# Optimization experiments

Measured on AMD Instinct MI355X. Metric: run time of the kernel, lower is better.

## Reference

```python
import jax, jax.numpy as jnp
import numpy as np

D = 2048          # in_features == out_features (d_model)
H_TOTAL = 8192    # hidden_features, split across experts
E = 8             # num_experts
K = 2             # num_selects (top-k)
HE = H_TOTAL // E # per-expert hidden size
B, S = 2, 2048


def setup_inputs() -> dict:
    key = jax.random.key(0)
    ks = jax.random.split(key, 8)
    scale_up = 1.0 / np.sqrt(D)
    scale_dn = 1.0 / np.sqrt(HE)
    return {
        "x": jax.random.normal(ks[0], (B, S, D), dtype=jnp.float32),
        # mlp gate network: Linear(D,E,no bias) -> tanh -> Linear(E,E,no bias)
        "Wg1": jax.random.normal(ks[1], (E, D), dtype=jnp.float32) * 0.02,
        "Wg2": jax.random.normal(ks[2], (E, E), dtype=jnp.float32) * 0.2,
        # per-expert GLU-MLP weights (stacked over expert axis)
        "Wup": jax.random.uniform(ks[3], (E, HE, D), dtype=jnp.float32, minval=-scale_up, maxval=scale_up),
        "bup": jax.random.uniform(ks[4], (E, HE), dtype=jnp.float32, minval=-scale_up, maxval=scale_up),
        "Wdown": jax.random.uniform(ks[5], (E, D, HE), dtype=jnp.float32, minval=-scale_dn, maxval=scale_dn),
        "bdown": jax.random.uniform(ks[6], (E, D), dtype=jnp.float32, minval=-scale_dn, maxval=scale_dn),
    }


def reference(x, Wg1, Wg2, Wup, bup, Wdown, bdown):
    Bd, Sd, Dd = x.shape
    T = Bd * Sd
    xt = x.reshape(T, Dd)                                   # [T, D] tokens

    # ---- TopKBalancedNoisyGate (eval mode: no noise) ----
    logits = jnp.tanh(xt @ Wg1.T) @ Wg2.T                   # [T, E]
    _, top_idx = jax.lax.top_k(logits, K)                   # [T, K]
    top_logits = jnp.take_along_axis(logits, top_idx, axis=1)
    top_scores = jax.nn.softmax(top_logits.astype(jnp.float32), axis=1).astype(logits.dtype)
    # scatter top-k scores into dense [T, E] (zeros elsewhere)
    rows = jnp.arange(T)[:, None]
    scores = jnp.zeros_like(logits).at[rows, top_idx].set(top_scores)

    # ---- per-expert Linear-GLU experts: up -> silu -> down, score-combined ----
    up = jnp.einsum('td,ehd->teh', xt, Wup) + bup           # [T, E, HE]
    h = jax.nn.silu(up)
    down = jnp.einsum('teh,eoh->teo', h, Wdown) + bdown     # [T, E, D]
    out = jnp.einsum('te,teo->to', scores, down)            # [T, D]
    return out.reshape(Bd, Sd, Dd)
```

## Files before the change

kernel.cpp:

```cpp
#include <hip/hip_runtime.h>
#include <hip/hip_bf16.h>

#define D_DIM 2048
#define HE_DIM 1024
#define E_NUM 8
#define T_NUM 4096
#define TK_NUM 8192
#define TILE 128
#define BK 64
#define MAXROWS 9216
#define MAXMT 72

#define M_CNT(e)  ((e) * 32)
#define M_FILL(e) (256 + (e) * 32)
#define M_OFF  512
#define M_NMT  520
#define M_TE   528
#define M_TB   600
#define M_TICKET 704
#define M_INTS 1024

typedef unsigned short u16;
typedef __attribute__((ext_vector_type(8))) short bf16x8;
typedef __attribute__((ext_vector_type(4))) float f32x4;

#define OFF_XB   ((size_t)0)
#define OFF_WUPB (OFF_XB + (size_t)T_NUM * D_DIM * 2)
#define OFF_SLOT ((size_t)0)
#define OFF_WDNB (OFF_WUPB + (size_t)E_NUM * HE_DIM * D_DIM * 2)
#define OFF_H    (OFF_WDNB + (size_t)E_NUM * D_DIM * HE_DIM * 2)
#define OFF_SCR  (OFF_H + (size_t)MAXROWS * HE_DIM * 2)
#define OFF_EIDX (OFF_SCR + (size_t)TK_NUM * 4)
#define OFF_RT   (OFF_EIDX + (size_t)TK_NUM * 4)
#define OFF_RS   (OFF_RT + (size_t)MAXROWS * 4)
#define OFF_META (OFF_RS + (size_t)MAXROWS * 4)

__device__ __forceinline__ u16 f2bf(float f) {
  unsigned u = __float_as_uint(f);
  u += 0x7FFFu + ((u >> 16) & 1u);
  return (u16)(u >> 16);
}
__device__ __forceinline__ float bf_lo(unsigned u) { return __uint_as_float(u << 16); }
__device__ __forceinline__ float bf_hi(unsigned u) { return __uint_as_float(u & 0xFFFF0000u); }

__device__ __forceinline__ void gload16(const void* g, void* l) {
  __builtin_amdgcn_global_load_lds((const __attribute__((address_space(1))) void*)g,
                                   (__attribute__((address_space(3))) void*)l,
                                   16, 0, 0);
}

#define WAIT_VM4 asm volatile("s_waitcnt vmcnt(4)" ::: "memory")
#define WAIT_VM0 asm volatile("s_waitcnt vmcnt(0)" ::: "memory")
#define SBAR     { __builtin_amdgcn_s_barrier(); asm volatile("" ::: "memory"); }

__global__ void k_cvt2(const float4* __restrict__ s1, const float4* __restrict__ s2,
                       ushort4* __restrict__ d1, ushort4* __restrict__ d2, int n4,
                       int* __restrict__ meta, int* __restrict__ rows_slot,
                       float* __restrict__ rowscore) {
  const int i0 = blockIdx.x * blockDim.x + threadIdx.x;
  if (i0 < M_INTS) meta[i0] = 0;
  if (i0 < MAXROWS) { rows_slot[i0] = -1; rowscore[i0] = 0.0f; }
  const int st = gridDim.x * blockDim.x;
  for (int i = i0; i < 2 * n4; i += st) {
    const float4* s = (i < n4) ? s1 : s2;
    ushort4* d = (i < n4) ? d1 : d2;
    int j = (i < n4) ? i : i - n4;
    float4 v = s[j];
    ushort4 o;
    o.x = f2bf(v.x); o.y = f2bf(v.y); o.z = f2bf(v.z); o.w = f2bf(v.w);
    d[j] = o;
  }
}

__global__ __launch_bounds__(256) void k_gate(
    const float4* __restrict__ x4, const float4* __restrict__ Wg1_4,
    const float* __restrict__ Wg2, ushort4* __restrict__ xb4,
    int* __restrict__ eidx, float* __restrict__ scr, int* __restrict__ meta) {
  __shared__ float4 wg1s[E_NUM * (D_DIM / 4)];
  __shared__ int cnt_s[E_NUM];
  __shared__ int lastf;
  const int tid = threadIdx.x;
  if (tid < E_NUM) cnt_s[tid] = 0;
#pragma unroll
  for (int i = 0; i < 16; ++i) wg1s[tid + i * 256] = Wg1_4[tid + i * 256];
  __syncthreads();

  const int w = tid >> 6;
  const int lane = tid & 63;
  for (int j = 0; j < 4; ++j) {
    const int t = blockIdx.x * 16 + w * 4 + j;
    float acc[E_NUM];
#pragma unroll
    for (int e = 0; e < E_NUM; ++e) acc[e] = 0.f;
#pragma unroll
    for (int i = 0; i < 8; ++i) {
      const int c = lane + i * 64;
      float4 xv = x4[(size_t)t * 512 + c];
      ushort4 o;
      o.x = f2bf(xv.x); o.y = f2bf(xv.y); o.z = f2bf(xv.z); o.w = f2bf(xv.w);
      xb4[(size_t)t * 512 + c] = o;
#pragma unroll
      for (int e = 0; e < E_NUM; ++e) {
        float4 wv = wg1s[e * 512 + c];
        acc[e] += xv.x * wv.x + xv.y * wv.y + xv.z * wv.z + xv.w * wv.w;
      }
    }
#pragma unroll
    for (int e = 0; e < E_NUM; ++e) {
      float v = acc[e];
#pragma unroll
      for (int off = 32; off; off >>= 1) v += __shfl_xor(v, off, 64);
      acc[e] = v;
    }
    if (lane == 0) {
      float l1[E_NUM], lg[E_NUM];
#pragma unroll
      for (int e = 0; e < E_NUM; ++e) l1[e] = tanhf(acc[e]);
#pragma unroll
      for (int i = 0; i < E_NUM; ++i) {
        float s = 0.f;
#pragma unroll
        for (int e = 0; e < E_NUM; ++e) s += l1[e] * Wg2[i * E_NUM + e];
        lg[i] = s;
      }
      int i0 = 0; float v0 = lg[0];
#pragma unroll
      for (int i = 1; i < E_NUM; ++i) if (lg[i] > v0) { v0 = lg[i]; i0 = i; }
      int i1 = -1; float v1 = -3.4e38f;
#pragma unroll
      for (int i = 0; i < E_NUM; ++i) if (i != i0 && lg[i] > v1) { v1 = lg[i]; i1 = i; }
      float e1 = __expf(v1 - v0);
      float s0 = 1.f / (1.f + e1);
      float s1 = e1 * s0;
      eidx[t * 2] = i0; eidx[t * 2 + 1] = i1;
      scr[t * 2] = s0;  scr[t * 2 + 1] = s1;
      atomicAdd(&cnt_s[i0], 1);
      atomicAdd(&cnt_s[i1], 1);
    }
  }
  __syncthreads();
  if (tid < E_NUM) atomicAdd(&meta[M_CNT(tid)], cnt_s[tid]);

  if (tid == 0) {
    __threadfence();
    lastf = (atomicAdd(&meta[M_TICKET], 1) == (int)gridDim.x - 1);
  }
  __syncthreads();
  if (lastf && tid < 64) {
    const int l2 = tid;
    int cnt = (l2 < E_NUM) ? atomicAdd(&meta[M_CNT(l2)], 0) : 0;
    int tiles = (cnt + TILE - 1) / TILE;
    int pre = tiles;
#pragma unroll
    for (int off = 1; off < E_NUM; off <<= 1) {
      int v = __shfl_up(pre, off, 64);
      if (l2 >= off && l2 < E_NUM) pre += v;
    }
    int tb_excl = pre - tiles;
    if (l2 < E_NUM) meta[M_OFF + l2] = tb_excl * TILE;
    const int nmt = __shfl(pre, E_NUM - 1, 64);
    if (l2 == 0) meta[M_NMT] = nmt;
    int tb[E_NUM];
#pragma unroll
    for (int k = 0; k < E_NUM; ++k) tb[k] = __shfl(tb_excl, k, 64);
    for (int mt = l2; mt < nmt; mt += 64) {
      int e = 0;
#pragma unroll
      for (int k = 1; k < E_NUM; ++k) if (mt >= tb[k]) e = k;
      meta[M_TE + mt] = e;
      meta[M_TB + mt] = mt * TILE;
    }
  }
}

__global__ void k_assign(const int* __restrict__ eidx, const float* __restrict__ scr,
                         int* __restrict__ meta, int* __restrict__ rows_slot,
                         float* __restrict__ rowscore) {
  int i = blockIdx.x * blockDim.x + threadIdx.x;
  const int lane = threadIdx.x & 63;
  int e = eidx[i];
  int pos = 0;
#pragma unroll
  for (int ex = 0; ex < E_NUM; ++ex) {
    unsigned long long m = __ballot(e == ex);
    if (e == ex) {
      int leader = __ffsll((long long)m) - 1;
      int rank = __popcll(m & ((1ull << lane) - 1ull));
      int b = 0;
      if (lane == leader) b = atomicAdd(&meta[M_FILL(ex)], __popcll(m));
      b = __shfl(b, leader, 64);
      pos = b + rank;
    }
  }
  int r = meta[M_OFF + e] + pos;
  rows_slot[r] = i;
  rowscore[r] = scr[i];
}

__global__ __launch_bounds__(512) void k_up(
    const u16* __restrict__ xb, const u16* __restrict__ wupb,
    const float* __restrict__ bup, const int* __restrict__ meta,
    const int* __restrict__ rows_slot, u16* __restrict__ hbuf) {
  const int mt = blockIdx.y;
  if (mt >= meta[M_NMT]) return;
  const int e = meta[M_TE + mt];
  const int mbase = meta[M_TB + mt];
  const int nt = blockIdx.x;

  __shared__ u16 As[3][TILE * BK];
  __shared__ u16 Bs[3][TILE * BK];

  const int tid = threadIdx.x;
  const int lane = tid & 63;
  const int w = tid >> 6;
  const int r0 = tid >> 3;
  const int cb = (((tid & 7) ^ (r0 & 7)) * 8);

  const u16* gA[2];
  const u16* gB[2];
#pragma unroll
  for (int j = 0; j < 2; ++j) {
    int s = rows_slot[mbase + r0 + 64 * j]; if (s < 0) s = 0;
    gA[j] = xb + (size_t)(s >> 1) * D_DIM + cb;
    gB[j] = wupb + ((size_t)e * HE_DIM + nt * TILE + r0 + 64 * j) * D_DIM + cb;
  }

  const int wm = (w & 1) * 64;
  const int wn = (w >> 1) * 32;
  const int quad = lane >> 4;
  const int l16 = lane & 15;
  const int sw = l16 & 7;

  f32x4 acc[4][2] = {};

#define STAGE_UP(buf, k0) \
  { gload16(gA[0] + (k0), &As[buf][tid * 8]);        \
    gload16(gA[1] + (k0), &As[buf][tid * 8 + 4096]); \
    gload16(gB[0] + (k0), &Bs[buf][tid * 8]);        \
    gload16(gB[1] + (k0), &Bs[buf][tid * 8 + 4096]); }

  STAGE_UP(0, 0);
  STAGE_UP(1, BK);
  WAIT_VM4;
  SBAR;
  int cur = 0, nxt = 2;
  for (int k0 = 0; k0 < D_DIM; k0 += BK) {
    const bool pf = (k0 + 2 * BK < D_DIM);
    if (pf) STAGE_UP(nxt, k0 + 2 * BK);
    const u16* pa0 = &As[cur][(wm + l16) * BK];
    const u16* pb0 = &Bs[cur][(wn + l16) * BK];
#pragma unroll
    for (int h = 0; h < 2; ++h) {
      const int off = ((h * 4 + quad) ^ sw) * 8;
      bf16x8 af[4], bfr[2];
#pragma unroll
      for (int i = 0; i < 4; ++i) af[i] = *(const bf16x8*)(pa0 + i * 16 * BK + off);
#pragma unroll
      for (int i = 0; i < 2; ++i) bfr[i] = *(const bf16x8*)(pb0 + i * 16 * BK + off);
#pragma unroll
      for (int mi = 0; mi < 4; ++mi)
#pragma unroll
        for (int ni = 0; ni < 2; ++ni)
          acc[mi][ni] = __builtin_amdgcn_mfma_f32_16x16x32_bf16(af[mi], bfr[ni], acc[mi][ni], 0, 0, 0);
    }
    if (pf) { WAIT_VM4; } else { WAIT_VM0; }
    SBAR;
    cur = (cur == 2) ? 0 : cur + 1;
    nxt = (nxt == 2) ? 0 : nxt + 1;
  }

#pragma unroll
  for (int mi = 0; mi < 4; ++mi) {
    const int m = wm + mi * 16 + quad * 4;
#pragma unroll
    for (int ni = 0; ni < 2; ++ni) {
      const int ng = nt * TILE + wn + ni * 16 + l16;
      const float bias = bup[e * HE_DIM + ng];
#pragma unroll
      for (int r = 0; r < 4; ++r) {
        float v = acc[mi][ni][r] + bias;
        v = v / (1.0f + __expf(-v));
        hbuf[(size_t)(mbase + m + r) * HE_DIM + ng] = f2bf(v);
      }
    }
  }
}

__global__ __launch_bounds__(512) void k_down(
    const u16* __restrict__ hbuf, const u16* __restrict__ wdnb,
    const float* __restrict__ bdown, const int* __restrict__ meta,
    const int* __restrict__ rows_slot, const float* __restrict__ rowscore,
    u16* __restrict__ slot) {
  const int mt = blockIdx.y;
  if (mt >= meta[M_NMT]) return;
  const int e = meta[M_TE + mt];
  const int mbase = meta[M_TB + mt];
  const int nt = blockIdx.x;

  __shared__ u16 As[3][TILE * BK];
  __shared__ u16 Bs[3][TILE * BK];

  const int tid = threadIdx.x;
  const int lane = tid & 63;
  const int w = tid >> 6;
  const int r0 = tid >> 3;
  const int cb = (((tid & 7) ^ (r0 & 7)) * 8);

  const u16* gA[2];
  const u16* gB[2];
#pragma unroll
  for (int j = 0; j < 2; ++j) {
    gA[j] = hbuf + (size_t)(mbase + r0 + 64 * j) * HE_DIM + cb;
    gB[j] = wdnb + ((size_t)e * D_DIM + nt * TILE + r0 + 64 * j) * HE_DIM + cb;
  }

  const int wm = (w & 1) * 64;
  const int wn = (w >> 1) * 32;
  const int quad = lane >> 4;
  const int l16 = lane & 15;
  const int sw = l16 & 7;

  f32x4 acc[4][2] = {};

#define STAGE_DN(buf, k0) \
  { gload16(gA[0] + (k0), &As[buf][tid * 8]);        \
    gload16(gA[1] + (k0), &As[buf][tid * 8 + 4096]); \
    gload16(gB[0] + (k0), &Bs[buf][tid * 8]);        \
    gload16(gB[1] + (k0), &Bs[buf][tid * 8 + 4096]); }

  STAGE_DN(0, 0);
  STAGE_DN(1, BK);
  WAIT_VM4;
  SBAR;
  int cur = 0, nxt = 2;
  for (int k0 = 0; k0 < HE_DIM; k0 += BK) {
    const bool pf = (k0 + 2 * BK < HE_DIM);
    if (pf) STAGE_DN(nxt, k0 + 2 * BK);
    const u16* pa0 = &As[cur][(wm + l16) * BK];
    const u16* pb0 = &Bs[cur][(wn + l16) * BK];
#pragma unroll
    for (int h = 0; h < 2; ++h) {
      const int off = ((h * 4 + quad) ^ sw) * 8;
      bf16x8 af[4], bfr[2];
#pragma unroll
      for (int i = 0; i < 4; ++i) af[i] = *(const bf16x8*)(pa0 + i * 16 * BK + off);
#pragma unroll
      for (int i = 0; i < 2; ++i) bfr[i] = *(const bf16x8*)(pb0 + i * 16 * BK + off);
#pragma unroll
      for (int mi = 0; mi < 4; ++mi)
#pragma unroll
        for (int ni = 0; ni < 2; ++ni)
          acc[mi][ni] = __builtin_amdgcn_mfma_f32_16x16x32_bf16(af[mi], bfr[ni], acc[mi][ni], 0, 0, 0);
    }
    if (pf) { WAIT_VM4; } else { WAIT_VM0; }
    SBAR;
    cur = (cur == 2) ? 0 : cur + 1;
    nxt = (nxt == 2) ? 0 : nxt + 1;
  }

#pragma unroll
  for (int mi = 0; mi < 4; ++mi) {
    const int m = wm + mi * 16 + quad * 4;
#pragma unroll
    for (int r = 0; r < 4; ++r) {
      const int rg = mbase + m + r;
      const int s = rows_slot[rg];
      const float sc = rowscore[rg];
      if (s < 0) continue;
      u16* dst = slot + (size_t)s * D_DIM;
#pragma unroll
      for (int ni = 0; ni < 2; ++ni) {
        const int ng = nt * TILE + wn + ni * 16 + l16;
        float v = (acc[mi][ni][r] + bdown[e * D_DIM + ng]) * sc;
        dst[ng] = f2bf(v);
      }
    }
  }
}

__global__ __launch_bounds__(256) void k_combine(const u16* __restrict__ slot,
                                                 float* __restrict__ out) {
  int i = blockIdx.x * blockDim.x + threadIdx.x;
  int t = i >> 8;
  int c = i & 255;
  const uint4* p0 = (const uint4*)(slot + (size_t)(t * 2) * D_DIM) + c;
  const uint4* p1 = (const uint4*)(slot + (size_t)(t * 2 + 1) * D_DIM) + c;
  uint4 a = *p0, b = *p1;
  float4 o0, o1;
  o0.x = bf_lo(a.x) + bf_lo(b.x);  o0.y = bf_hi(a.x) + bf_hi(b.x);
  o0.z = bf_lo(a.y) + bf_lo(b.y);  o0.w = bf_hi(a.y) + bf_hi(b.y);
  o1.x = bf_lo(a.z) + bf_lo(b.z);  o1.y = bf_hi(a.z) + bf_hi(b.z);
  o1.z = bf_lo(a.w) + bf_lo(b.w);  o1.w = bf_hi(a.w) + bf_hi(b.w);
  float4* po = (float4*)(out + (size_t)t * D_DIM) + c * 2;
  po[0] = o0;
  po[1] = o1;
}

extern "C" void kernel_launch(void* const* d_in, const int* in_sizes, int n_in,
                              void* d_out, int out_size, void* d_ws, size_t ws_size,
                              hipStream_t stream) {
  const float* x     = (const float*)d_in[0];
  const float* Wg1   = (const float*)d_in[1];
  const float* Wg2   = (const float*)d_in[2];
  const float* Wup   = (const float*)d_in[3];
  const float* bup   = (const float*)d_in[4];
  const float* Wdown = (const float*)d_in[5];
  const float* bdown = (const float*)d_in[6];
  float* out = (float*)d_out;

  char* ws = (char*)d_ws;
  u16*   xb         = (u16*)(ws + OFF_XB);
  u16*   wupb       = (u16*)(ws + OFF_WUPB);
  u16*   wdnb       = (u16*)(ws + OFF_WDNB);
  u16*   hbuf       = (u16*)(ws + OFF_H);
  u16*   slotbuf    = (u16*)(ws + OFF_SLOT);
  float* scr        = (float*)(ws + OFF_SCR);
  int*   eidx       = (int*)(ws + OFF_EIDX);
  int*   rows_slot  = (int*)(ws + OFF_RT);
  float* rowscore   = (float*)(ws + OFF_RS);
  int*   meta       = (int*)(ws + OFF_META);

  k_cvt2<<<8192, 256, 0, stream>>>((const float4*)Wup, (const float4*)Wdown,
                                   (ushort4*)wupb, (ushort4*)wdnb,
                                   E_NUM * HE_DIM * D_DIM / 4,
                                   meta, rows_slot, rowscore);
  k_gate<<<T_NUM / 16, 256, 0, stream>>>((const float4*)x, (const float4*)Wg1, Wg2,
                                         (ushort4*)xb, eidx, scr, meta);
  k_assign<<<TK_NUM / 256, 256, 0, stream>>>(eidx, scr, meta, rows_slot, rowscore);
  k_up<<<dim3(HE_DIM / TILE, MAXMT), 512, 0, stream>>>(xb, wupb, bup, meta, rows_slot, hbuf);
  k_down<<<dim3(D_DIM / TILE, MAXMT), 512, 0, stream>>>(hbuf, wdnb, bdown, meta,
                                                        rows_slot, rowscore, slotbuf);
  k_combine<<<T_NUM * D_DIM / 8 / 256, 256, 0, stream>>>(slotbuf, out);
}
```

Before: 420.7 us.

## Use 4-wave blocks with 64x64 warp tiles and BK=32 in expert GEMMs

Both expert GEMM kernels go from 8 waves to 4 waves per 128x128 block, so each wave now computes a 64x64 sub-tile (4x4 MFMAs) instead of 64x32. The K step drops from 64 to 32, the global-to-LDS loader is remapped for 256 threads with a matching 4-way XOR swizzle, and s_setprio is raised around the MFMA burst. The aim is more register-level reuse per fragment load, less LDS traffic per FLOP, and smaller LDS footprint for higher occupancy. In exchange there are twice as many loop iterations and barriers per K, and higher accumulator register pressure.

```diff
diff --git a/kernel.cpp b/kernel.cpp
--- a/kernel.cpp
+++ b/kernel.cpp
@@ -7,7 +7,7 @@
 #define T_NUM 4096
 #define TK_NUM 8192
 #define TILE 128
-#define BK 64
+#define BK 32
 #define MAXROWS 9216
 #define MAXMT 72
 
@@ -197,7 +197,7 @@
   rowscore[r] = scr[i];
 }
 
-__global__ __launch_bounds__(512) void k_up(
+__global__ __launch_bounds__(256) void k_up(
     const u16* __restrict__ xb, const u16* __restrict__ wupb,
     const float* __restrict__ bup, const int* __restrict__ meta,
     const int* __restrict__ rows_slot, u16* __restrict__ hbuf) {
@@ -213,8 +213,8 @@
   const int tid = threadIdx.x;
   const int lane = tid & 63;
   const int w = tid >> 6;
-  const int r0 = tid >> 3;
-  const int cb = (((tid & 7) ^ (r0 & 7)) * 8);
+  const int r0 = tid >> 2;
+  const int cb = (((tid & 3) ^ ((r0 >> 2) & 3)) * 8);
 
   const u16* gA[2];
   const u16* gB[2];
@@ -226,54 +226,54 @@
   }
 
   const int wm = (w & 1) * 64;
-  const int wn = (w >> 1) * 32;
+  const int wn = (w >> 1) * 64;
   const int quad = lane >> 4;
   const int l16 = lane & 15;
-  const int sw = l16 & 7;
-
-  f32x4 acc[4][2] = {};
+  const int koff = ((quad ^ (l16 >> 2)) & 3) * 8;
+
+  f32x4 acc[4][4] = {};
 
 #define STAGE_UP(buf, k0) \
   { gload16(gA[0] + (k0), &As[buf][tid * 8]);        \
-    gload16(gA[1] + (k0), &As[buf][tid * 8 + 4096]); \
+    gload16(gA[1] + (k0), &As[buf][tid * 8 + 2048]); \
     gload16(gB[0] + (k0), &Bs[buf][tid * 8]);        \
-    gload16(gB[1] + (k0), &Bs[buf][tid * 8 + 4096]); }
+    gload16(gB[1] + (k0), &Bs[buf][tid * 8 + 2048]); }
 
   STAGE_UP(0, 0);
   STAGE_UP(1, BK);
   WAIT_VM4;
   SBAR;
-  int cur = 0, nxt = 2;
-  for (int k0 = 0; k0 < D_DIM; k0 += BK) {
-    const bool pf = (k0 + 2 * BK < D_DIM);
-    if (pf) STAGE_UP(nxt, k0 + 2 * BK);
-    const u16* pa0 = &As[cur][(wm + l16) * BK];
-    const u16* pb0 = &Bs[cur][(wn + l16) * BK];
-#pragma unroll
-    for (int h = 0; h < 2; ++h) {
-      const int off = ((h * 4 + quad) ^ sw) * 8;
-      bf16x8 af[4], bfr[2];
-#pragma unroll
-      for (int i = 0; i < 4; ++i) af[i] = *(const bf16x8*)(pa0 + i * 16 * BK + off);
-#pragma unroll
-      for (int i = 0; i < 2; ++i) bfr[i] = *(const bf16x8*)(pb0 + i * 16 * BK + off);
-#pragma unroll
-      for (int mi = 0; mi < 4; ++mi)
-#pragma unroll
-        for (int ni = 0; ni < 2; ++ni)
-          acc[mi][ni] = __builtin_amdgcn_mfma_f32_16x16x32_bf16(af[mi], bfr[ni], acc[mi][ni], 0, 0, 0);
-    }
+  int cur = 0;
+  const int NT = D_DIM / BK;
+  for (int t = 0; t < NT; ++t) {
+    const bool pf = (t + 2 < NT);
+    const int nxt = (cur == 0) ? 2 : cur - 1;
+    if (pf) STAGE_UP(nxt, (t + 2) * BK);
+    const u16* pa0 = &As[cur][(wm + l16) * BK + koff];
+    const u16* pb0 = &Bs[cur][(wn + l16) * BK + koff];
+    bf16x8 af[4], bfr[4];
+#pragma unroll
+    for (int i = 0; i < 4; ++i) {
+      af[i]  = *(const bf16x8*)(pa0 + i * 16 * BK);
+      bfr[i] = *(const bf16x8*)(pb0 + i * 16 * BK);
+    }
+    __builtin_amdgcn_s_setprio(1);
+#pragma unroll
+    for (int mi = 0; mi < 4; ++mi)
+#pragma unroll
+      for (int ni = 0; ni < 4; ++ni)
+        acc[mi][ni] = __builtin_amdgcn_mfma_f32_16x16x32_bf16(af[mi], bfr[ni], acc[mi][ni], 0, 0, 0);
+    __builtin_amdgcn_s_setprio(0);
     if (pf) { WAIT_VM4; } else { WAIT_VM0; }
     SBAR;
     cur = (cur == 2) ? 0 : cur + 1;
-    nxt = (nxt == 2) ? 0 : nxt + 1;
   }
 
 #pragma unroll
   for (int mi = 0; mi < 4; ++mi) {
     const int m = wm + mi * 16 + quad * 4;
 #pragma unroll
-    for (int ni = 0; ni < 2; ++ni) {
+    for (int ni = 0; ni < 4; ++ni) {
       const int ng = nt * TILE + wn + ni * 16 + l16;
       const float bias = bup[e * HE_DIM + ng];
 #pragma unroll
@@ -286,7 +286,7 @@
   }
 }
 
-__global__ __launch_bounds__(512) void k_down(
+__global__ __launch_bounds__(256) void k_down(
     const u16* __restrict__ hbuf, const u16* __restrict__ wdnb,
     const float* __restrict__ bdown, const int* __restrict__ meta,
     const int* __restrict__ rows_slot, const float* __restrict__ rowscore,
@@ -303,8 +303,8 @@
   const int tid = threadIdx.x;
   const int lane = tid & 63;
   const int w = tid >> 6;
-  const int r0 = tid >> 3;
-  const int cb = (((tid & 7) ^ (r0 & 7)) * 8);
+  const int r0 = tid >> 2;
+  const int cb = (((tid & 3) ^ ((r0 >> 2) & 3)) * 8);
 
   const u16* gA[2];
   const u16* gB[2];
@@ -315,47 +315,47 @@
   }
 
   const int wm = (w & 1) * 64;
-  const int wn = (w >> 1) * 32;
+  const int wn = (w >> 1) * 64;
   const int quad = lane >> 4;
   const int l16 = lane & 15;
-  const int sw = l16 & 7;
-
-  f32x4 acc[4][2] = {};
+  const int koff = ((quad ^ (l16 >> 2)) & 3) * 8;
+
+  f32x4 acc[4][4] = {};
 
 #define STAGE_DN(buf, k0) \
   { gload16(gA[0] + (k0), &As[buf][tid * 8]);        \
-    gload16(gA[1] + (k0), &As[buf][tid * 8 + 4096]); \
+    gload16(gA[1] + (k0), &As[buf][tid * 8 + 2048]); \
     gload16(gB[0] + (k0), &Bs[buf][tid * 8]);        \
-    gload16(gB[1] + (k0), &Bs[buf][tid * 8 + 4096]); }
+    gload16(gB[1] + (k0), &Bs[buf][tid * 8 + 2048]); }
 
   STAGE_DN(0, 0);
   STAGE_DN(1, BK);
   WAIT_VM4;
   SBAR;
-  int cur = 0, nxt = 2;
-  for (int k0 = 0; k0 < HE_DIM; k0 += BK) {
-    const bool pf = (k0 + 2 * BK < HE_DIM);
-    if (pf) STAGE_DN(nxt, k0 + 2 * BK);
-    const u16* pa0 = &As[cur][(wm + l16) * BK];
-    const u16* pb0 = &Bs[cur][(wn + l16) * BK];
-#pragma unroll
-    for (int h = 0; h < 2; ++h) {
-      const int off = ((h * 4 + quad) ^ sw) * 8;
-      bf16x8 af[4], bfr[2];
-#pragma unroll
-      for (int i = 0; i < 4; ++i) af[i] = *(const bf16x8*)(pa0 + i * 16 * BK + off);
-#pragma unroll
-      for (int i = 0; i < 2; ++i) bfr[i] = *(const bf16x8*)(pb0 + i * 16 * BK + off);
-#pragma unroll
-      for (int mi = 0; mi < 4; ++mi)
-#pragma unroll
-        for (int ni = 0; ni < 2; ++ni)
-          acc[mi][ni] = __builtin_amdgcn_mfma_f32_16x16x32_bf16(af[mi], bfr[ni], acc[mi][ni], 0, 0, 0);
-    }
+  int cur = 0;
+  const int NT = HE_DIM / BK;
+  for (int t = 0; t < NT; ++t) {
+    const bool pf = (t + 2 < NT);
+    const int nxt = (cur == 0) ? 2 : cur - 1;
+    if (pf) STAGE_DN(nxt, (t + 2) * BK);
+    const u16* pa0 = &As[cur][(wm + l16) * BK + koff];
+    const u16* pb0 = &Bs[cur][(wn + l16) * BK + koff];
+    bf16x8 af[4], bfr[4];
+#pragma unroll
+    for (int i = 0; i < 4; ++i) {
+      af[i]  = *(const bf16x8*)(pa0 + i * 16 * BK);
+      bfr[i] = *(const bf16x8*)(pb0 + i * 16 * BK);
+    }
+    __builtin_amdgcn_s_setprio(1);
+#pragma unroll
+    for (int mi = 0; mi < 4; ++mi)
+#pragma unroll
+      for (int ni = 0; ni < 4; ++ni)
+        acc[mi][ni] = __builtin_amdgcn_mfma_f32_16x16x32_bf16(af[mi], bfr[ni], acc[mi][ni], 0, 0, 0);
+    __builtin_amdgcn_s_setprio(0);
     if (pf) { WAIT_VM4; } else { WAIT_VM0; }
     SBAR;
     cur = (cur == 2) ? 0 : cur + 1;
-    nxt = (nxt == 2) ? 0 : nxt + 1;
   }
 
 #pragma unroll
@@ -369,7 +369,7 @@
       if (s < 0) continue;
       u16* dst = slot + (size_t)s * D_DIM;
 #pragma unroll
-      for (int ni = 0; ni < 2; ++ni) {
+      for (int ni = 0; ni < 4; ++ni) {
         const int ng = nt * TILE + wn + ni * 16 + l16;
         float v = (acc[mi][ni][r] + bdown[e * D_DIM + ng]) * sc;
         dst[ng] = f2bf(v);
@@ -427,8 +427,8 @@
   k_gate<<<T_NUM / 16, 256, 0, stream>>>((const float4*)x, (const float4*)Wg1, Wg2,
                                          (ushort4*)xb, eidx, scr, meta);
   k_assign<<<TK_NUM / 256, 256, 0, stream>>>(eidx, scr, meta, rows_slot, rowscore);
-  k_up<<<dim3(HE_DIM / TILE, MAXMT), 512, 0, stream>>>(xb, wupb, bup, meta, rows_slot, hbuf);
-  k_down<<<dim3(D_DIM / TILE, MAXMT), 512, 0, stream>>>(hbuf, wdnb, bdown, meta,
+  k_up<<<dim3(HE_DIM / TILE, MAXMT), 256, 0, stream>>>(xb, wupb, bup, meta, rows_slot, hbuf);
+  k_down<<<dim3(D_DIM / TILE, MAXMT), 256, 0, stream>>>(hbuf, wdnb, bdown, meta,
                                                         rows_slot, rowscore, slotbuf);
   k_combine<<<T_NUM * D_DIM / 8 / 256, 256, 0, stream>>>(slotbuf, out);
 }
```

New measurement: 403.1 us. -4.2%, faster.
